# Optimization experiments

Hardware: AMD Instinct MI355X
Metric: run time of the kernel (lower is better)

## Reference

```python
import jax, jax.numpy as jnp
import numpy as np

N_NODES = 10000
N_CHANNELS = 32
DIM = 3
N_LAYERS = 2
BASIS_R = 2   # basis_rank_max
FEAT_R = 2    # feature_rank_max
NU_MAX = 3
N_EDGES = 160000


def setup_inputs() -> dict:
    key = jax.random.key(0)
    ks = jax.random.split(key, 8)
    pos = jax.random.normal(ks[0], (N_NODES, DIM), jnp.float32)
    edge_index = jax.random.randint(ks[1], (2, N_EDGES), 0, N_NODES, dtype=jnp.int32)
    atoms = jnp.zeros((N_NODES,), jnp.int32)  # Embedding(1, C) -> all indices 0
    emb_w = jax.random.normal(ks[2], (1, N_CHANNELS), jnp.float32)
    W_ab = 0.1 * jax.random.normal(ks[3], (N_LAYERS, BASIS_R + 1, FEAT_R + 1, N_CHANNELS, N_CHANNELS), jnp.float32)
    ws_w = 0.1 * jax.random.normal(ks[4], (N_LAYERS, FEAT_R + 1, NU_MAX, N_CHANNELS), jnp.float32)
    channel_w = 0.1 * jax.random.normal(ks[5], (N_LAYERS, FEAT_R + 1, N_NODES, N_CHANNELS, N_CHANNELS), jnp.float32)
    message_w = 0.1 * jax.random.normal(ks[6], (N_LAYERS, FEAT_R + 1, N_NODES, N_CHANNELS, N_CHANNELS), jnp.float32)
    return dict(pos=pos, edge_index=edge_index, atoms=atoms, emb_w=emb_w,
                W_ab=W_ab, ws_w=ws_w, channel_w=channel_w, message_w=message_w)


def _u_powers(u, max_rank):
    # u: (E, DIM) unit vectors; returns [u^{\otimes k}] flattened to (E, DIM**k)
    pows = [jnp.ones((u.shape[0], 1), u.dtype)]
    for _ in range(max_rank):
        pows.append((pows[-1][:, :, None] * u[:, None, :]).reshape(u.shape[0], -1))
    return pows


def reference(pos, edge_index, atoms, emb_w, W_ab, ws_w, channel_w, message_w):
    src, dst = edge_index[0], edge_index[1]
    rel = pos[dst] - pos[src]                                   # (E, 3)
    u = rel / (jnp.linalg.norm(rel, axis=-1, keepdims=True) + 1e-9)
    u_pow = _u_powers(u, max(BASIS_R, FEAT_R))

    # node features h[c]: (N, C, 3**c) (trailing Cartesian indices flattened)
    h = [jnp.zeros((N_NODES, N_CHANNELS, DIM ** c), pos.dtype) for c in range(FEAT_R + 1)]
    h[0] = h[0] + emb_w[atoms][:, :, None]

    for l in range(N_LAYERS):
        # ---- atomic basis: A_c(i) = sum_{j->i} sum_a W^{(c,a)} (h_a(j) . u^{ox a}) u^{ox c}
        A = []
        for c in range(BASIS_R + 1):
            acc = jnp.zeros((N_EDGES, N_CHANNELS), pos.dtype)
            for a in range(FEAT_R + 1):
                s = jnp.einsum('ecd,ed->ec', h[a][src], u_pow[a])   # full contraction -> scalar
                acc = acc + jnp.einsum('jk,ek->ej', W_ab[l, c, a], s)
            contrib = acc[:, :, None] * u_pow[c][:, None, :]        # (E, C, 3**c)
            A.append(jax.ops.segment_sum(contrib, dst, num_segments=N_NODES))
        # ---- weighted sum (product basis): m_c = sum_nu w_{c,nu} (A_0)^{nu-1} A_c
        s0 = A[0][..., 0]                                           # (N, C)
        messages = []
        for c in range(FEAT_R + 1):
            m = jnp.zeros_like(A[c])
            p = jnp.ones_like(s0)
            for nu in range(NU_MAX):
                m = m + ws_w[l, c, nu][None, :, None] * (p[:, :, None] * A[c])
                p = p * s0
            messages.append(m)
        # ---- update (MACE eq. 11): per-node channel mixing of old state + messages
        h = [jnp.einsum('ijk,ikd->ijd', channel_w[l, c], h[c])
             + jnp.einsum('ijk,ikd->ijd', message_w[l, c], messages[c])
             for c in range(FEAT_R + 1)]

    # concatenate ranks along flattened Cartesian axis: (N, C, 1+3+9)
    return jnp.concatenate(h, axis=-1)
```

## Files before the change

kernel.cpp:

```cpp
#include <hip/hip_runtime.h>

#define N_NODES 10000
#define N_CH    32
#define N_EDGES 160000
#define HPAD    16
#define SLOTS   8

__device__ __forceinline__ float dot4(float4 a, float4 b) {
    return a.x*b.x + a.y*b.y + a.z*b.z + a.w*b.w;
}

__global__ void k_hist(const int* __restrict__ ei, int* __restrict__ deg) {
    int e = blockIdx.x * 256 + threadIdx.x;
    atomicAdd(&deg[ei[N_EDGES + e]], 1);
}

__global__ __launch_bounds__(1024) void k_scan(const int* __restrict__ deg,
                                               int* __restrict__ offs,
                                               int* __restrict__ cursor) {
    __shared__ int part[1024];
    const int t = threadIdx.x;
    const int base = t * 10;
    int s = 0;
#pragma unroll
    for (int r = 0; r < 10; ++r) { int i = base + r; if (i < N_NODES) s += deg[i]; }
    part[t] = s;
    __syncthreads();
    for (int off = 1; off < 1024; off <<= 1) {
        int v = (t >= off) ? part[t - off] : 0;
        __syncthreads();
        part[t] += v;
        __syncthreads();
    }
    int run = (t > 0) ? part[t - 1] : 0;
#pragma unroll
    for (int r = 0; r < 10; ++r) {
        int i = base + r;
        if (i < N_NODES) { offs[i] = run; cursor[i] = run; run += deg[i]; }
    }
    if (t == 0) offs[N_NODES] = N_EDGES;
}

__global__ void k_scatter(const int* __restrict__ ei, const float* __restrict__ pos,
                          int* __restrict__ cursor, int* __restrict__ ssrc,
                          float4* __restrict__ us4) {
    int e = blockIdx.x * 256 + threadIdx.x;
    int s = ei[e], d = ei[N_EDGES + e];
    float rx = pos[d*3+0] - pos[s*3+0];
    float ry = pos[d*3+1] - pos[s*3+1];
    float rz = pos[d*3+2] - pos[s*3+2];
    float inv = 1.0f / (sqrtf(rx*rx + ry*ry + rz*rz) + 1e-9f);
    int p = atomicAdd(&cursor[d], 1);
    ssrc[p] = s;
    us4[p] = make_float4(rx*inv, ry*inv, rz*inv, 0.f);
}

__global__ __launch_bounds__(256) void k_gather(
    const int layer,
    const float* __restrict__ hPrev,
    const float* __restrict__ emb_w,
    const int* __restrict__ ssrc,
    const float4* __restrict__ us4,
    const int* __restrict__ offs,
    const float* __restrict__ W_ab,
    const float* __restrict__ ws_w,
    float* __restrict__ msgd)
{
    __shared__ __align__(16) float Tlds[SLOTS * 3 * 10 * 32];
    __shared__ __align__(16) float Wlds[3 * 32 * 36];

    const int slot = threadIdx.x >> 5;
    const int j    = threadIdx.x & 31;
    const int node = blockIdx.x * SLOTS + slot;

    const int e0 = offs[node], e1 = offs[node + 1];
    const int aMax = (layer == 0) ? 1 : 3;

    float T0[10], T1[10], T2[10];
#pragma unroll
    for (int d = 0; d < 10; ++d) { T0[d] = 0.f; T1[d] = 0.f; T2[d] = 0.f; }

    if (layer == 0) {
        float U[10];
#pragma unroll
        for (int d = 0; d < 10; ++d) U[d] = 0.f;
        for (int idx = e0; idx < e1; ++idx) {
            const float4 u = us4[idx];
            U[0] += 1.f;
            U[1] += u.x;      U[2] += u.y;      U[3] += u.z;
            U[4] += u.x*u.x;  U[5] += u.x*u.y;  U[6] += u.x*u.z;
            U[7] += u.y*u.y;  U[8] += u.y*u.z;  U[9] += u.z*u.z;
        }
        const float s0 = emb_w[j];
#pragma unroll
        for (int d = 0; d < 10; ++d) T0[d] = s0 * U[d];
    } else {
        for (int idx = e0; idx < e1; ++idx) {
            const int src = ssrc[idx];
            const float4 u = us4[idx];
            const float* hr = hPrev + ((size_t)(src * N_CH + j)) * HPAD;
            const float4 a0 = *(const float4*)(hr);
            const float4 a1 = *(const float4*)(hr + 4);
            const float4 a2 = *(const float4*)(hr + 8);
            const float h12 = hr[12];

            const float xx = u.x*u.x, xy = u.x*u.y, xz = u.x*u.z;
            const float yy = u.y*u.y, yz = u.y*u.z, zz = u.z*u.z;
            float up[10];
            up[0] = 1.f; up[1] = u.x; up[2] = u.y; up[3] = u.z;
            up[4] = xx; up[5] = xy; up[6] = xz; up[7] = yy; up[8] = yz; up[9] = zz;

            const float s0 = a0.x;
            const float s1 = a0.y*u.x + a0.z*u.y + a0.w*u.z;
            const float s2 = a1.x*xx + (a1.y + a1.w)*xy + (a1.z + a2.z)*xz
                           + a2.x*yy + (a2.y + a2.w)*yz + h12*zz;
#pragma unroll
            for (int d = 0; d < 10; ++d) {
                T0[d] += s0 * up[d];
                T1[d] += s1 * up[d];
                T2[d] += s2 * up[d];
            }
        }
    }

#pragma unroll
    for (int d = 0; d < 10; ++d)
        Tlds[((slot * 3 + 0) * 10 + d) * 32 + j] = T0[d];
    if (layer != 0) {
#pragma unroll
        for (int d = 0; d < 10; ++d) {
            Tlds[((slot * 3 + 1) * 10 + d) * 32 + j] = T1[d];
            Tlds[((slot * 3 + 2) * 10 + d) * 32 + j] = T2[d];
        }
    }

    float acc[10];
#pragma unroll
    for (int d = 0; d < 10; ++d) acc[d] = 0.f;

#pragma unroll
    for (int c = 0; c < 3; ++c) {
        __syncthreads();
        const float* wsrc = W_ab + ((size_t)((layer * 3 + c) * 3)) * 1024;
        for (int t = threadIdx.x; t < 3072; t += 256) {
            int a = t >> 10, rem = t & 1023;
            Wlds[a * 1152 + (rem >> 5) * 36 + (rem & 31)] = wsrc[t];
        }
        __syncthreads();
        const int dlo = (c == 0) ? 0 : ((c == 1) ? 1 : 4);
        const int dhi = (c == 0) ? 1 : ((c == 1) ? 4 : 10);
        for (int a = 0; a < aMax; ++a) {
            const float* wrow = Wlds + a * 1152 + j * 36;
#pragma unroll
            for (int k4 = 0; k4 < 8; ++k4) {
                const float4 w4 = *(const float4*)(wrow + k4 * 4);
                for (int d = dlo; d < dhi; ++d) {
                    const float4 t4 = *(const float4*)&Tlds[((slot * 3 + a) * 10 + d) * 32 + k4 * 4];
                    acc[d] += dot4(w4, t4);
                }
            }
        }
    }

    const float s0n = acc[0];
    const float s0sq = s0n * s0n;
    float poly[3];
#pragma unroll
    for (int c = 0; c < 3; ++c) {
        const float* wsp = ws_w + ((size_t)((layer * 3 + c) * 3)) * 32 + j;
        poly[c] = wsp[0] + wsp[32] * s0n + wsp[64] * s0sq;
    }
#pragma unroll
    for (int d = 0; d < 10; ++d) {
        const float p = (d == 0) ? poly[0] : ((d < 4) ? poly[1] : poly[2]);
        msgd[((size_t)node * 10 + d) * 32 + j] = p * acc[d];
    }
}

__global__ __launch_bounds__(256) void k_update(
    const int layer,
    const float* __restrict__ hPrev,
    const float* __restrict__ emb_w,
    const float* __restrict__ msgd,
    const float* __restrict__ cw,
    const float* __restrict__ mw,
    float* __restrict__ hOut,
    const int outStride)
{
    __shared__ __align__(16) float hls[SLOTS * 13 * 32];
    __shared__ __align__(16) float mls[SLOTS * 13 * 32];

    const int slot = threadIdx.x >> 5;
    const int j    = threadIdx.x & 31;
    const int node = blockIdx.x * SLOTS + slot;

    if (layer == 0) {
        hls[(slot * 13 + 0) * 32 + j] = emb_w[j];
#pragma unroll
        for (int m = 1; m < 13; ++m) hls[(slot * 13 + m) * 32 + j] = 0.f;
    } else {
        const float* hr = hPrev + ((size_t)(node * N_CH + j)) * HPAD;
        const float4 a0 = *(const float4*)(hr);
        const float4 a1 = *(const float4*)(hr + 4);
        const float4 a2 = *(const float4*)(hr + 8);
        const float h12 = hr[12];
        const float hv[13] = {a0.x, a0.y, a0.z, a0.w, a1.x, a1.y, a1.z, a1.w,
                              a2.x, a2.y, a2.z, a2.w, h12};
#pragma unroll
        for (int m = 0; m < 13; ++m) hls[(slot * 13 + m) * 32 + j] = hv[m];
    }

    {
        float md[10];
#pragma unroll
        for (int d = 0; d < 10; ++d) md[d] = msgd[((size_t)node * 10 + d) * 32 + j];
        const int mExp[13] = {0, 1, 2, 3, 4, 5, 6, 5, 7, 8, 6, 8, 9};
#pragma unroll
        for (int m = 0; m < 13; ++m) mls[(slot * 13 + m) * 32 + j] = md[mExp[m]];
    }
    __syncthreads();

    float out[13];
#pragma unroll
    for (int m = 0; m < 13; ++m) out[m] = 0.f;

#pragma unroll
    for (int c = 0; c < 3; ++c) {
        const int mlo = (c == 0) ? 0 : ((c == 1) ? 1 : 4);
        const int mhi = (c == 0) ? 1 : ((c == 1) ? 4 : 13);
        const size_t wb = (((size_t)(layer * 3 + c) * N_NODES + node) * 32 + j) * 32;
        const float4* cwr = (const float4*)(cw + wb);
        const float4* mwr = (const float4*)(mw + wb);
#pragma unroll
        for (int k4 = 0; k4 < 8; ++k4) {
            const float4 c4 = cwr[k4];
            const float4 m4 = mwr[k4];
            for (int m = mlo; m < mhi; ++m) {
                out[m] += dot4(c4, *(const float4*)&hls[(slot * 13 + m) * 32 + k4 * 4])
                        + dot4(m4, *(const float4*)&mls[(slot * 13 + m) * 32 + k4 * 4]);
            }
        }
    }

    float* orow = hOut + ((size_t)(node * N_CH + j)) * outStride;
#pragma unroll
    for (int m = 0; m < 13; ++m) orow[m] = out[m];
}

extern "C" void kernel_launch(void* const* d_in, const int* in_sizes, int n_in,
                              void* d_out, int out_size, void* d_ws, size_t ws_size,
                              hipStream_t stream) {
    const float* pos   = (const float*)d_in[0];
    const int*   ei    = (const int*)d_in[1];
    const float* emb_w = (const float*)d_in[3];
    const float* W_ab  = (const float*)d_in[4];
    const float* ws_w  = (const float*)d_in[5];
    const float* cw    = (const float*)d_in[6];
    const float* mw    = (const float*)d_in[7];
    float* out = (float*)d_out;

    char* ws = (char*)d_ws;
    float* hB   = (float*)ws; ws += (size_t)N_NODES * N_CH * HPAD * 4;
    float4* us4 = (float4*)ws; ws += (size_t)N_EDGES * 16;
    float* msgd = (float*)ws; ws += (size_t)N_NODES * 10 * 32 * 4;
    int* ssrc   = (int*)ws;   ws += (size_t)N_EDGES * 4;
    int* offs   = (int*)ws;   ws += (size_t)(N_NODES + 16) * 4;
    int* cursor = (int*)ws;   ws += (size_t)N_NODES * 4;
    int* deg    = (int*)ws;   ws += (size_t)N_NODES * 4;

    hipMemsetAsync(deg, 0, N_NODES * 4, stream);
    k_hist<<<N_EDGES / 256, 256, 0, stream>>>(ei, deg);
    k_scan<<<1, 1024, 0, stream>>>(deg, offs, cursor);
    k_scatter<<<N_EDGES / 256, 256, 0, stream>>>(ei, pos, cursor, ssrc, us4);

    k_gather<<<N_NODES / SLOTS, 256, 0, stream>>>(0, (const float*)nullptr, emb_w,
                                                  ssrc, us4, offs, W_ab, ws_w, msgd);
    k_update<<<N_NODES / SLOTS, 256, 0, stream>>>(0, (const float*)nullptr, emb_w,
                                                  msgd, cw, mw, hB, HPAD);
    k_gather<<<N_NODES / SLOTS, 256, 0, stream>>>(1, hB, emb_w,
                                                  ssrc, us4, offs, W_ab, ws_w, msgd);
    k_update<<<N_NODES / SLOTS, 256, 0, stream>>>(1, hB, emb_w,
                                                  msgd, cw, mw, out, 13);
}
```

Baseline: 724.0 us.

## Fuse gather and update kernels per layer and specialize layer 0 via template

Merges the per-layer gather (edge aggregation plus W_ab mixing) and update (per-node channel mixing) kernels into one templated kernel, so messages stay in shared memory instead of going through a global msgd buffer. Layer 0 is specialized at compile time: it loads only one W_ab slice, skips the channel_w loads for ranks 1 and 2 because h is zero there, and uses smaller shared buffers. The edge loop is unrolled by 2. The cost is one extra barrier and more shared-memory aliasing inside a single longer kernel.

```diff
diff --git a/kernel.cpp b/kernel.cpp
--- a/kernel.cpp
+++ b/kernel.cpp
@@ -55,8 +55,8 @@
     us4[p] = make_float4(rx*inv, ry*inv, rz*inv, 0.f);
 }
 
-__global__ __launch_bounds__(256) void k_gather(
-    const int layer,
+template<int LAYER>
+__global__ __launch_bounds__(256) void k_fused(
     const float* __restrict__ hPrev,
     const float* __restrict__ emb_w,
     const int* __restrict__ ssrc,
@@ -64,23 +64,30 @@
     const int* __restrict__ offs,
     const float* __restrict__ W_ab,
     const float* __restrict__ ws_w,
-    float* __restrict__ msgd)
+    const float* __restrict__ cw,
+    const float* __restrict__ mw,
+    float* __restrict__ hOut,
+    const int outStride)
 {
-    __shared__ __align__(16) float Tlds[SLOTS * 3 * 10 * 32];
-    __shared__ __align__(16) float Wlds[3 * 32 * 36];
+    constexpr int AMAX = (LAYER == 0) ? 1 : 3;
+    constexpr int TSZ   = SLOTS * AMAX * 10 * 32;
+    constexpr int MSZ   = SLOTS * 13 * 32;
+    constexpr int HSZ   = (LAYER == 0) ? 32 : MSZ;
+    constexpr int BUFSZ = (TSZ > MSZ + HSZ) ? TSZ : (MSZ + HSZ);
+    __shared__ __align__(16) float buf[BUFSZ];
+    __shared__ __align__(16) float Wlds[AMAX * 32 * 36];
+
+    float* Tlds = buf;
+    float* hls  = buf;
+    float* mls  = buf + HSZ;
 
     const int slot = threadIdx.x >> 5;
     const int j    = threadIdx.x & 31;
     const int node = blockIdx.x * SLOTS + slot;
 
     const int e0 = offs[node], e1 = offs[node + 1];
-    const int aMax = (layer == 0) ? 1 : 3;
-
-    float T0[10], T1[10], T2[10];
-#pragma unroll
-    for (int d = 0; d < 10; ++d) { T0[d] = 0.f; T1[d] = 0.f; T2[d] = 0.f; }
-
-    if (layer == 0) {
+
+    if (LAYER == 0) {
         float U[10];
 #pragma unroll
         for (int d = 0; d < 10; ++d) U[d] = 0.f;
@@ -93,8 +100,13 @@
         }
         const float s0 = emb_w[j];
 #pragma unroll
-        for (int d = 0; d < 10; ++d) T0[d] = s0 * U[d];
+        for (int d = 0; d < 10; ++d)
+            Tlds[(slot * 10 + d) * 32 + j] = s0 * U[d];
     } else {
+        float T0[10], T1[10], T2[10];
+#pragma unroll
+        for (int d = 0; d < 10; ++d) { T0[d] = 0.f; T1[d] = 0.f; T2[d] = 0.f; }
+#pragma unroll 2
         for (int idx = e0; idx < e1; ++idx) {
             const int src = ssrc[idx];
             const float4 u = us4[idx];
@@ -121,14 +133,9 @@
                 T2[d] += s2 * up[d];
             }
         }
-    }
-
-#pragma unroll
-    for (int d = 0; d < 10; ++d)
-        Tlds[((slot * 3 + 0) * 10 + d) * 32 + j] = T0[d];
-    if (layer != 0) {
 #pragma unroll
         for (int d = 0; d < 10; ++d) {
+            Tlds[((slot * 3 + 0) * 10 + d) * 32 + j] = T0[d];
             Tlds[((slot * 3 + 1) * 10 + d) * 32 + j] = T1[d];
             Tlds[((slot * 3 + 2) * 10 + d) * 32 + j] = T2[d];
         }
@@ -141,63 +148,48 @@
 #pragma unroll
     for (int c = 0; c < 3; ++c) {
         __syncthreads();
-        const float* wsrc = W_ab + ((size_t)((layer * 3 + c) * 3)) * 1024;
-        for (int t = threadIdx.x; t < 3072; t += 256) {
+        const float* wsrc = W_ab + ((size_t)((LAYER * 3 + c) * 3)) * 1024;
+        for (int t = threadIdx.x; t < AMAX * 1024; t += 256) {
             int a = t >> 10, rem = t & 1023;
             Wlds[a * 1152 + (rem >> 5) * 36 + (rem & 31)] = wsrc[t];
         }
         __syncthreads();
         const int dlo = (c == 0) ? 0 : ((c == 1) ? 1 : 4);
         const int dhi = (c == 0) ? 1 : ((c == 1) ? 4 : 10);
-        for (int a = 0; a < aMax; ++a) {
+#pragma unroll
+        for (int a = 0; a < AMAX; ++a) {
             const float* wrow = Wlds + a * 1152 + j * 36;
 #pragma unroll
             for (int k4 = 0; k4 < 8; ++k4) {
                 const float4 w4 = *(const float4*)(wrow + k4 * 4);
                 for (int d = dlo; d < dhi; ++d) {
-                    const float4 t4 = *(const float4*)&Tlds[((slot * 3 + a) * 10 + d) * 32 + k4 * 4];
+                    const float4 t4 = *(const float4*)&Tlds[((slot * AMAX + a) * 10 + d) * 32 + k4 * 4];
                     acc[d] += dot4(w4, t4);
                 }
             }
         }
     }
+    __syncthreads();
 
     const float s0n = acc[0];
     const float s0sq = s0n * s0n;
     float poly[3];
 #pragma unroll
     for (int c = 0; c < 3; ++c) {
-        const float* wsp = ws_w + ((size_t)((layer * 3 + c) * 3)) * 32 + j;
+        const float* wsp = ws_w + ((size_t)((LAYER * 3 + c) * 3)) * 32 + j;
         poly[c] = wsp[0] + wsp[32] * s0n + wsp[64] * s0sq;
     }
-#pragma unroll
-    for (int d = 0; d < 10; ++d) {
-        const float p = (d == 0) ? poly[0] : ((d < 4) ? poly[1] : poly[2]);
-        msgd[((size_t)node * 10 + d) * 32 + j] = p * acc[d];
-    }
-}
-
-__global__ __launch_bounds__(256) void k_update(
-    const int layer,
-    const float* __restrict__ hPrev,
-    const float* __restrict__ emb_w,
-    const float* __restrict__ msgd,
-    const float* __restrict__ cw,
-    const float* __restrict__ mw,
-    float* __restrict__ hOut,
-    const int outStride)
-{
-    __shared__ __align__(16) float hls[SLOTS * 13 * 32];
-    __shared__ __align__(16) float mls[SLOTS * 13 * 32];
-
-    const int slot = threadIdx.x >> 5;
-    const int j    = threadIdx.x & 31;
-    const int node = blockIdx.x * SLOTS + slot;
-
-    if (layer == 0) {
-        hls[(slot * 13 + 0) * 32 + j] = emb_w[j];
-#pragma unroll
-        for (int m = 1; m < 13; ++m) hls[(slot * 13 + m) * 32 + j] = 0.f;
+    {
+        const int mExp[13] = {0, 1, 2, 3, 4, 5, 6, 5, 7, 8, 6, 8, 9};
+#pragma unroll
+        for (int m = 0; m < 13; ++m) {
+            const float p = (m == 0) ? poly[0] : ((m < 4) ? poly[1] : poly[2]);
+            mls[(slot * 13 + m) * 32 + j] = p * acc[mExp[m]];
+        }
+    }
+
+    if (LAYER == 0) {
+        if (threadIdx.x < 32) hls[threadIdx.x] = emb_w[threadIdx.x];
     } else {
         const float* hr = hPrev + ((size_t)(node * N_CH + j)) * HPAD;
         const float4 a0 = *(const float4*)(hr);
@@ -209,15 +201,6 @@
 #pragma unroll
         for (int m = 0; m < 13; ++m) hls[(slot * 13 + m) * 32 + j] = hv[m];
     }
-
-    {
-        float md[10];
-#pragma unroll
-        for (int d = 0; d < 10; ++d) md[d] = msgd[((size_t)node * 10 + d) * 32 + j];
-        const int mExp[13] = {0, 1, 2, 3, 4, 5, 6, 5, 7, 8, 6, 8, 9};
-#pragma unroll
-        for (int m = 0; m < 13; ++m) mls[(slot * 13 + m) * 32 + j] = md[mExp[m]];
-    }
     __syncthreads();
 
     float out[13];
@@ -228,16 +211,36 @@
     for (int c = 0; c < 3; ++c) {
         const int mlo = (c == 0) ? 0 : ((c == 1) ? 1 : 4);
         const int mhi = (c == 0) ? 1 : ((c == 1) ? 4 : 13);
-        const size_t wb = (((size_t)(layer * 3 + c) * N_NODES + node) * 32 + j) * 32;
-        const float4* cwr = (const float4*)(cw + wb);
+        const size_t wb = (((size_t)(LAYER * 3 + c) * N_NODES + node) * 32 + j) * 32;
         const float4* mwr = (const float4*)(mw + wb);
-#pragma unroll
-        for (int k4 = 0; k4 < 8; ++k4) {
-            const float4 c4 = cwr[k4];
-            const float4 m4 = mwr[k4];
-            for (int m = mlo; m < mhi; ++m) {
-                out[m] += dot4(c4, *(const float4*)&hls[(slot * 13 + m) * 32 + k4 * 4])
-                        + dot4(m4, *(const float4*)&mls[(slot * 13 + m) * 32 + k4 * 4]);
+        if (LAYER == 0) {
+            if (c == 0) {
+                const float4* cwr = (const float4*)(cw + wb);
+#pragma unroll
+                for (int k4 = 0; k4 < 8; ++k4) {
+                    const float4 c4 = cwr[k4];
+                    const float4 m4 = mwr[k4];
+                    out[0] += dot4(c4, *(const float4*)&hls[k4 * 4])
+                            + dot4(m4, *(const float4*)&mls[(slot * 13) * 32 + k4 * 4]);
+                }
+            } else {
+#pragma unroll
+                for (int k4 = 0; k4 < 8; ++k4) {
+                    const float4 m4 = mwr[k4];
+                    for (int m = mlo; m < mhi; ++m)
+                        out[m] += dot4(m4, *(const float4*)&mls[(slot * 13 + m) * 32 + k4 * 4]);
+                }
+            }
+        } else {
+            const float4* cwr = (const float4*)(cw + wb);
+#pragma unroll
+            for (int k4 = 0; k4 < 8; ++k4) {
+                const float4 c4 = cwr[k4];
+                const float4 m4 = mwr[k4];
+                for (int m = mlo; m < mhi; ++m) {
+                    out[m] += dot4(c4, *(const float4*)&hls[(slot * 13 + m) * 32 + k4 * 4])
+                            + dot4(m4, *(const float4*)&mls[(slot * 13 + m) * 32 + k4 * 4]);
+                }
             }
         }
     }
@@ -260,25 +263,20 @@
     float* out = (float*)d_out;
 
     char* ws = (char*)d_ws;
-    float* hB   = (float*)ws; ws += (size_t)N_NODES * N_CH * HPAD * 4;
+    float* hB   = (float*)ws;  ws += (size_t)N_NODES * N_CH * HPAD * 4;
     float4* us4 = (float4*)ws; ws += (size_t)N_EDGES * 16;
-    float* msgd = (float*)ws; ws += (size_t)N_NODES * 10 * 32 * 4;
-    int* ssrc   = (int*)ws;   ws += (size_t)N_EDGES * 4;
-    int* offs   = (int*)ws;   ws += (size_t)(N_NODES + 16) * 4;
-    int* cursor = (int*)ws;   ws += (size_t)N_NODES * 4;
-    int* deg    = (int*)ws;   ws += (size_t)N_NODES * 4;
+    int* ssrc   = (int*)ws;    ws += (size_t)N_EDGES * 4;
+    int* offs   = (int*)ws;    ws += (size_t)(N_NODES + 16) * 4;
+    int* cursor = (int*)ws;    ws += (size_t)N_NODES * 4;
+    int* deg    = (int*)ws;    ws += (size_t)N_NODES * 4;
 
     hipMemsetAsync(deg, 0, N_NODES * 4, stream);
     k_hist<<<N_EDGES / 256, 256, 0, stream>>>(ei, deg);
     k_scan<<<1, 1024, 0, stream>>>(deg, offs, cursor);
     k_scatter<<<N_EDGES / 256, 256, 0, stream>>>(ei, pos, cursor, ssrc, us4);
 
-    k_gather<<<N_NODES / SLOTS, 256, 0, stream>>>(0, (const float*)nullptr, emb_w,
-                                                  ssrc, us4, offs, W_ab, ws_w, msgd);
-    k_update<<<N_NODES / SLOTS, 256, 0, stream>>>(0, (const float*)nullptr, emb_w,
-                                                  msgd, cw, mw, hB, HPAD);
-    k_gather<<<N_NODES / SLOTS, 256, 0, stream>>>(1, hB, emb_w,
-                                                  ssrc, us4, offs, W_ab, ws_w, msgd);
-    k_update<<<N_NODES / SLOTS, 256, 0, stream>>>(1, hB, emb_w,
-                                                  msgd, cw, mw, out, 13);
-}
+    k_fused<0><<<N_NODES / SLOTS, 256, 0, stream>>>(nullptr, emb_w, ssrc, us4, offs,
+                                                    W_ab, ws_w, cw, mw, hB, HPAD);
+    k_fused<1><<<N_NODES / SLOTS, 256, 0, stream>>>(hB, emb_w, ssrc, us4, offs,
+                                                    W_ab, ws_w, cw, mw, out, 13);
+}
```

Result: faster. 699.7 us (-3.4%).
